# Kernel optimization log

Measured on AMD Instinct MI355X. Metric: run time of the kernel, lower is better.

The kernel has to match this reference:

```python
import jax, jax.numpy as jnp
import numpy as np

B, L, D, H = 2, 2048, 512, 8
DH = D // H
THRESHOLD = 0.1


def setup_inputs() -> dict:
    key = jax.random.key(0)
    ks = jax.random.split(key, 8)
    s = 0.02  # weight scale to keep activations sane
    return {
        "q_x": jax.random.normal(ks[0], (B, L, D), jnp.float32),
        "k_x": jax.random.normal(ks[1], (B, L, D), jnp.float32),
        "v_x": jax.random.normal(ks[2], (B, L, D), jnp.float32),
        "energy_coeffs": jax.random.normal(ks[3], (B, L, 16), jnp.float32),
        "Wq": jax.random.normal(ks[4], (D, D), jnp.float32) * s,
        "bq": jnp.zeros((D,), jnp.float32),
        "Wk": jax.random.normal(ks[5], (D, D), jnp.float32) * s,
        "bk": jnp.zeros((D,), jnp.float32),
        "Wv": jax.random.normal(ks[6], (D, D), jnp.float32) * s,
        "bv": jnp.zeros((D,), jnp.float32),
        "Wo": jax.random.normal(ks[7], (D, D), jnp.float32) * s,
        "bo": jnp.zeros((D,), jnp.float32),
    }


def reference(q_x, k_x, v_x, energy_coeffs, Wq, bq, Wk, bk, Wv, bv, Wo, bo):
    b, l, d = q_x.shape
    # QKV projections (torch Linear: x @ W.T + b), split heads -> [B,H,L,Dh]
    Q = (q_x @ Wq.T + bq).reshape(b, l, H, DH).transpose(0, 2, 1, 3)
    K = (k_x @ Wk.T + bk).reshape(b, -1, H, DH).transpose(0, 2, 1, 3)
    V = (v_x @ Wv.T + bv).reshape(b, -1, H, DH).transpose(0, 2, 1, 3)
    scores = jnp.einsum("bhqd,bhkd->bhqk", Q, K) / jnp.sqrt(jnp.float32(DH))
    # straight-through energy-based key mask
    energy = jnp.abs(energy_coeffs).mean(axis=-1)  # [B, Lk]
    soft = jax.nn.sigmoid((energy - THRESHOLD) * 10.0)
    hard = (energy > THRESHOLD).astype(q_x.dtype)
    mask_val = soft + jax.lax.stop_gradient(hard - soft)  # fwd=hard, grad=soft
    scores = scores + (1.0 - mask_val)[:, None, None, :] * (-1e9)
    attn = jax.nn.softmax(scores, axis=-1)
    out = jnp.einsum("bhqk,bhkd->bhqd", attn, V)
    out = out.transpose(0, 2, 1, 3).reshape(b, l, d)
    return out @ Wo.T + bo
```

## Files before the change

### kernel.cpp

```cpp
#include <hip/hip_runtime.h>
#include <stdint.h>

#define B_ 2
#define L_ 2048
#define D_ 512
#define H_ 8
#define DH_ 64

using frag8 = __attribute__((ext_vector_type(8))) short;
using bf4   = __attribute__((ext_vector_type(4))) short;
using f32x4 = __attribute__((ext_vector_type(4))) float;
using u32x4 = __attribute__((ext_vector_type(4))) unsigned int;

#define QSC 0.18033688011112042f

__device__ __forceinline__ unsigned short f2bf(float f) {
    unsigned int u = __float_as_uint(f);
    u += 0x7fffu + ((u >> 16) & 1u);
    return (unsigned short)(u >> 16);
}

__device__ __forceinline__ unsigned int cvtpk(float lo, float hi_) {
    unsigned int r;
    asm("v_cvt_pk_bf16_f32 %0, %1, %2" : "=v"(r) : "v"(lo), "v"(hi_));
    return r;
}

__device__ __forceinline__ void gl2lds16(const void* g, void* lds) {
    __builtin_amdgcn_global_load_lds((const __attribute__((address_space(1))) void*)g,
                                     (__attribute__((address_space(3))) void*)lds,
                                     16, 0, 0);
}

template<int N>
__device__ __forceinline__ void vmwait() {
    asm volatile("s_waitcnt vmcnt(%0)" :: "n"(N) : "memory");
}

__global__ __launch_bounds__(256) void cvt_mask_kernel(
    const float* __restrict__ qx, const float* __restrict__ kx, const float* __restrict__ vx,
    const float* __restrict__ Wq, const float* __restrict__ Wk, const float* __restrict__ Wv,
    const float* __restrict__ Wo, const float* __restrict__ ec,
    unsigned short* qb, unsigned short* kb, unsigned short* vb,
    unsigned short* wqb, unsigned short* wkb, unsigned short* wvb, unsigned short* wob,
    float* __restrict__ mk)
{
    const long NA = (long)B_ * L_ * D_;
    const long NW = (long)D_ * D_;
    const long total4 = (3 * NA + 4 * NW) / 4;
    long q4 = (long)blockIdx.x * 256 + threadIdx.x;
    if (q4 < total4) {
        long i = q4 * 4;
        const float* src; unsigned short* dst; long off;
        if (i < NA)            { src = qx; dst = qb; off = i; }
        else if (i < 2 * NA)   { src = kx; dst = kb; off = i - NA; }
        else if (i < 3 * NA)   { src = vx; dst = vb; off = i - 2 * NA; }
        else {
            long j = i - 3 * NA;
            int w = (int)(j / NW);
            off = j - (long)w * NW;
            src = (w == 0) ? Wq : (w == 1) ? Wk : (w == 2) ? Wv : Wo;
            dst = (w == 0) ? wqb : (w == 1) ? wkb : (w == 2) ? wvb : wob;
        }
        float4 v = *(const float4*)(src + off);
        ushort4 o;
        o.x = f2bf(v.x); o.y = f2bf(v.y); o.z = f2bf(v.z); o.w = f2bf(v.w);
        *(ushort4*)(dst + off) = o;
    } else {
        long i = q4 - total4;
        if (i < B_ * L_) {
            const float4* p4 = (const float4*)(ec + i * 16);
            float s = 0.0f;
#pragma unroll
            for (int j = 0; j < 4; ++j) {
                float4 v = p4[j];
                s += fabsf(v.x) + fabsf(v.y) + fabsf(v.z) + fabsf(v.w);
            }
            float energy = s * (1.0f / 16.0f);
            mk[i] = (energy > 0.1f) ? 0.0f : -1.0e9f;
        }
    }
}

struct GemmArgs { const unsigned short* A; const unsigned short* W;
                  const float* bias; void* C; int mode; };

template<int BM, int BN>
__global__ __launch_bounds__(256) void gemm_kernel(GemmArgs a0, GemmArgs a1, GemmArgs a2,
                                                   int M, int N, int K)
{
    const int nwg = gridDim.x * gridDim.y * gridDim.z;
    int flat = blockIdx.x + gridDim.x * (blockIdx.y + gridDim.y * blockIdx.z);
    int swz  = (flat & 7) * (nwg >> 3) + (flat >> 3);
    const int bx = swz % gridDim.x;
    int t2 = swz / gridDim.x;
    const int by = t2 % gridDim.y;
    const int bz = t2 / gridDim.y;

    GemmArgs ga = bz == 0 ? a0 : (bz == 1 ? a1 : a2);
    const unsigned short* __restrict__ A = ga.A;
    const unsigned short* __restrict__ W = ga.W;
    const float* __restrict__ bias = ga.bias;

    constexpr int MF = BM / 32;
    constexpr int NF = BN / 32;
    constexpr int NL = BM / 32 + BN / 32;

    __shared__ __align__(16) unsigned short As[2][BM * 64];
    __shared__ __align__(16) unsigned short Bs[2][BN * 64];

    const int tid  = threadIdx.x;
    const int lane = tid & 63;
    const int wave = tid >> 6;
    const int hi   = lane >> 4;
    const int ln   = lane & 15;
    const int wr   = wave >> 1;
    const int wc   = wave & 1;

    const long mBase = (long)by * BM;
    const long nBase = (long)bx * BN;

    f32x4 acc[MF][NF];
#pragma unroll
    for (int n = 0; n < NF; ++n) {
        float bv = bias[nBase + wc * (BN / 2) + n * 16 + ln];
#pragma unroll
        for (int m = 0; m < MF; ++m) acc[m][n] = (f32x4){bv, bv, bv, bv};
    }

#define GSTAGE(KT, BUF) do {                                                    \
    _Pragma("unroll")                                                           \
    for (int i_ = 0; i_ < BM / 32; ++i_) {                                      \
        int cl_ = i_ * 256 + tid;                                               \
        int r_ = cl_ >> 3, c_ = cl_ & 7, s_ = c_ ^ (r_ & 7);                    \
        gl2lds16(A + (mBase + r_) * K + (KT) + s_ * 8, As[BUF] + cl_ * 8);      \
    }                                                                           \
    _Pragma("unroll")                                                           \
    for (int i_ = 0; i_ < BN / 32; ++i_) {                                      \
        int cl_ = i_ * 256 + tid;                                               \
        int r_ = cl_ >> 3, c_ = cl_ & 7, s_ = c_ ^ (r_ & 7);                    \
        gl2lds16(W + (nBase + r_) * K + (KT) + s_ * 8, Bs[BUF] + cl_ * 8);      \
    }                                                                           \
} while (0)

    GSTAGE(0, 0);

    const int nk = K / 64;
    for (int t = 0; t < nk; ++t) {
        const int buf = t & 1;
        if (t + 1 < nk) {
            GSTAGE((t + 1) * 64, buf ^ 1);
            vmwait<NL>();
        } else {
            vmwait<0>();
        }
        __builtin_amdgcn_s_barrier();
        __builtin_amdgcn_sched_barrier(0);

        frag8 af[2][MF], bfr[2][NF];
#pragma unroll
        for (int kk = 0; kk < 2; ++kk) {
#pragma unroll
            for (int m = 0; m < MF; ++m) {
                int row = wr * (BM / 2) + m * 16 + ln;
                int c = (kk * 4 + hi) ^ (row & 7);
                af[kk][m] = *(const frag8*)(As[buf] + row * 64 + c * 8);
            }
#pragma unroll
            for (int n = 0; n < NF; ++n) {
                int row = wc * (BN / 2) + n * 16 + ln;
                int c = (kk * 4 + hi) ^ (row & 7);
                bfr[kk][n] = *(const frag8*)(Bs[buf] + row * 64 + c * 8);
            }
        }
        __builtin_amdgcn_s_setprio(1);
#pragma unroll
        for (int kk = 0; kk < 2; ++kk)
#pragma unroll
            for (int m = 0; m < MF; ++m)
#pragma unroll
                for (int n = 0; n < NF; ++n)
                    acc[m][n] = __builtin_amdgcn_mfma_f32_16x16x32_bf16(af[kk][m], bfr[kk][n], acc[m][n], 0, 0, 0);
        __builtin_amdgcn_s_setprio(0);
        __builtin_amdgcn_sched_barrier(0);
        __builtin_amdgcn_s_barrier();
    }
#undef GSTAGE

    const int mode = ga.mode;
#pragma unroll
    for (int m = 0; m < MF; ++m) {
#pragma unroll
        for (int n = 0; n < NF; ++n) {
            long col = nBase + wc * (BN / 2) + n * 16 + ln;
#pragma unroll
            for (int j = 0; j < 4; ++j) {
                long row = mBase + wr * (BM / 2) + m * 16 + hi * 4 + j;
                float v = acc[m][n][j];
                if (mode == 3) {
                    ((float*)ga.C)[row * N + col] = v;
                } else if (mode == 2) {
                    int dh = (int)col & 63;
                    int swv = ((dh & 7) << 1) | ((dh >> 3) & 1);
                    long nt = (row & ~63L) | (long)(((((int)(row >> 2)) & 15) ^ swv) << 2) | (row & 3);
                    ((unsigned short*)ga.C)[col * (long)(B_ * L_) + nt] = f2bf(v);
                } else {
                    if (mode == 1) v *= QSC;
                    ((unsigned short*)ga.C)[row * N + col] = f2bf(v);
                }
            }
        }
    }
}

__global__ __launch_bounds__(512, 4) void attn_kernel(
    const unsigned short* __restrict__ Qg, const unsigned short* __restrict__ Kg,
    const unsigned short* __restrict__ Vt, const float* __restrict__ mkg,
    unsigned short* __restrict__ Og)
{
    const int tid  = threadIdx.x;
    const int lane = tid & 63;
    const int wave = tid >> 6;
    const int grp  = wave >> 2;
    const int wq   = wave & 3;
    const int gtid = tid & 255;
    const int hi   = lane >> 4;
    const int ln   = lane & 15;

    const int bh = blockIdx.y;
    const int b  = bh >> 3, h = bh & 7;
    const unsigned short* Qb = Qg + ((long)b * L_) * D_ + h * DH_;
    const unsigned short* Kb = Kg + ((long)b * L_) * D_ + h * DH_;
    const unsigned short* Vb = Vt + (long)(h * DH_) * (B_ * L_) + (long)b * L_;
    const float* mkb = mkg + (long)b * L_;

    __shared__ __align__(16) char smem[65536];
    unsigned short* KsG = (unsigned short*)(smem + grp * 32768);
    unsigned short* VsG = (unsigned short*)(smem + grp * 32768 + 16384);

    const int q0 = blockIdx.x * 64 + wq * 16;

    frag8 qf[2];
#pragma unroll
    for (int ks = 0; ks < 2; ++ks)
        qf[ks] = *(const frag8*)(Qb + (long)(q0 + ln) * D_ + ks * 32 + hi * 8);

    const int sw  = ((ln & 7) << 1) | ((ln >> 3) & 1);
    const int sl0 = ((hi     ) ^ sw) << 2;
    const int sl1 = ((hi + 4 ) ^ sw) << 2;
    const int sl2 = ((hi + 8 ) ^ sw) << 2;
    const int sl3 = ((hi + 12) ^ sw) << 2;

#define STAGE(TT, BUF) do {                                                     \
    _Pragma("unroll")                                                           \
    for (int c2_ = 0; c2_ < 2; ++c2_) {                                         \
        int cl_ = c2_ * 256 + gtid;                                             \
        int r_ = cl_ >> 3, c_ = cl_ & 7;                                        \
        gl2lds16(Kb + (long)((TT) * 64 + r_) * D_ + ((c_ ^ (r_ & 7)) << 3),     \
                 KsG + (BUF) * 4096 + cl_ * 8);                                 \
        gl2lds16(Vb + (long)r_ * (B_ * L_) + (TT) * 64 + (c_ << 3),             \
                 VsG + (BUF) * 4096 + cl_ * 8);                                 \
    }                                                                           \
} while (0)

#define LOADM(TT, A0, A1, A2, A3) do {                                          \
    A0 = *(const f32x4*)(mkb + (TT) * 64 +      4 * hi);                        \
    A1 = *(const f32x4*)(mkb + (TT) * 64 + 16 + 4 * hi);                        \
    A2 = *(const f32x4*)(mkb + (TT) * 64 + 32 + 4 * hi);                        \
    A3 = *(const f32x4*)(mkb + (TT) * 64 + 48 + 4 * hi);                        \
} while (0)

    f32x4 o[4];
#pragma unroll
    for (int g = 0; g < 4; ++g) o[g] = (f32x4){0.f, 0.f, 0.f, 0.f};
    float m_run = -__builtin_inff();
    float l_run = 0.0f;
    f32x4 scp[4];
    f32x4 mc0, mc1, mc2, mc3;
    f32x4 mn0, mn1, mn2, mn3;

    auto SOFTPV = [&](const unsigned short* Vl) {
        float a0 = fmaxf(fmaxf(scp[0][0], scp[0][1]), fmaxf(scp[0][2], scp[0][3]));
        float a1 = fmaxf(fmaxf(scp[1][0], scp[1][1]), fmaxf(scp[1][2], scp[1][3]));
        float a2 = fmaxf(fmaxf(scp[2][0], scp[2][1]), fmaxf(scp[2][2], scp[2][3]));
        float a3 = fmaxf(fmaxf(scp[3][0], scp[3][1]), fmaxf(scp[3][2], scp[3][3]));
        float tl = fmaxf(fmaxf(a0, a1), fmaxf(a2, a3));
        float tA = __shfl_xor(tl, 16);
        float tB = __shfl_xor(tl, 32);
        float tC = __shfl_xor(tl, 48);
        float tmax = fmaxf(fmaxf(tl, tA), fmaxf(tB, tC));

        if (!__all(tmax <= m_run + 8.0f)) {
            float m_new = fmaxf(m_run, tmax);
            float alpha = __builtin_amdgcn_exp2f(m_run - m_new);
            float b0 = __shfl(alpha, 4 * hi + 0);
            float b1 = __shfl(alpha, 4 * hi + 1);
            float b2 = __shfl(alpha, 4 * hi + 2);
            float b3 = __shfl(alpha, 4 * hi + 3);
#pragma unroll
            for (int g = 0; g < 4; ++g) {
                o[g][0] *= b0; o[g][1] *= b1; o[g][2] *= b2; o[g][3] *= b3;
            }
            l_run *= alpha;
            m_run = m_new;
        }

        float p[16];
#pragma unroll
        for (int sh = 0; sh < 4; ++sh)
#pragma unroll
            for (int r = 0; r < 4; ++r)
                p[sh * 4 + r] = __builtin_amdgcn_exp2f(scp[sh][r] - m_run);
        float s01 = (p[0] + p[1]) + (p[2] + p[3]);
        float s23 = (p[4] + p[5]) + (p[6] + p[7]);
        float s45 = (p[8] + p[9]) + (p[10] + p[11]);
        float s67 = (p[12] + p[13]) + (p[14] + p[15]);
        float ps = (s01 + s23) + (s45 + s67);
        float pA = __shfl_xor(ps, 16);
        float pB = __shfl_xor(ps, 32);
        float pC = __shfl_xor(ps, 48);
        l_run += (ps + pA) + (pB + pC);

        union PU { u32x4 u; frag8 f; } p0u, p1u;
        p0u.u = (u32x4){cvtpk(p[0], p[1]),  cvtpk(p[2], p[3]),
                        cvtpk(p[4], p[5]),  cvtpk(p[6], p[7])};
        p1u.u = (u32x4){cvtpk(p[8], p[9]),  cvtpk(p[10], p[11]),
                        cvtpk(p[12], p[13]), cvtpk(p[14], p[15])};

        __builtin_amdgcn_s_setprio(1);
#pragma unroll
        for (int g = 0; g < 4; ++g) {
            int rowb = (g * 16 + ln) * 64;
            bf4 v0 = *(const bf4*)(Vl + rowb + sl0);
            bf4 v1 = *(const bf4*)(Vl + rowb + sl1);
            bf4 v2 = *(const bf4*)(Vl + rowb + sl2);
            bf4 v3 = *(const bf4*)(Vl + rowb + sl3);
            frag8 vf0 = __builtin_shufflevector(v0, v1, 0, 1, 2, 3, 4, 5, 6, 7);
            frag8 vf1 = __builtin_shufflevector(v2, v3, 0, 1, 2, 3, 4, 5, 6, 7);
            o[g] = __builtin_amdgcn_mfma_f32_16x16x32_bf16(p0u.f, vf0, o[g], 0, 0, 0);
            o[g] = __builtin_amdgcn_mfma_f32_16x16x32_bf16(p1u.f, vf1, o[g], 0, 0, 0);
        }
        __builtin_amdgcn_s_setprio(0);
    };

    auto QKSAVE = [&](const unsigned short* Kl) {
        scp[0] = mc0; scp[1] = mc1; scp[2] = mc2; scp[3] = mc3;
        __builtin_amdgcn_s_setprio(1);
#pragma unroll
        for (int sh = 0; sh < 4; ++sh) {
            int key = sh * 16 + ln;
#pragma unroll
            for (int ks = 0; ks < 2; ++ks) {
                frag8 kf = *(const frag8*)(Kl + key * 64 + (((ks * 4 + hi) ^ (ln & 7)) << 3));
                scp[sh] = __builtin_amdgcn_mfma_f32_16x16x32_bf16(kf, qf[ks], scp[sh], 0, 0, 0);
            }
        }
        __builtin_amdgcn_s_setprio(0);
    };

    STAGE(grp, 0);
    LOADM(grp, mc0, mc1, mc2, mc3);
    vmwait<0>();
    __builtin_amdgcn_s_barrier();
    __builtin_amdgcn_sched_barrier(0);
    STAGE(2 + grp, 1);
    LOADM(2 + grp, mn0, mn1, mn2, mn3);
    QKSAVE(KsG);

    for (int i = 1; i < 16; ++i) {
        const int buf = i & 1;
        SOFTPV(VsG + (buf ^ 1) * 4096);
        vmwait<0>();
        __builtin_amdgcn_s_barrier();
        __builtin_amdgcn_sched_barrier(0);
        if (i < 15) STAGE(2 * (i + 1) + grp, buf ^ 1);
        mc0 = mn0; mc1 = mn1; mc2 = mn2; mc3 = mn3;
        if (i < 15) LOADM(2 * (i + 1) + grp, mn0, mn1, mn2, mn3);
        QKSAVE(KsG + buf * 4096);
    }
    SOFTPV(VsG + 4096);
#undef STAGE
#undef LOADM

    __syncthreads();
    float* oX = (float*)smem;
    float* mX = (float*)(smem + 64 * 68 * 4);
    float* lX = mX + 64;

    if (grp == 1) {
#pragma unroll
        for (int g = 0; g < 4; ++g)
#pragma unroll
            for (int j = 0; j < 4; ++j)
                oX[(wq * 16 + 4 * hi + j) * 68 + g * 16 + ln] = o[g][j];
        if (hi == 0) { mX[wq * 16 + ln] = m_run; lX[wq * 16 + ln] = l_run; }
    }
    __syncthreads();
    if (grp == 0) {
#pragma unroll
        for (int j = 0; j < 4; ++j) {
            int q = 4 * hi + j;
            float mA = __shfl(m_run, q);
            float lA = __shfl(l_run, q);
            float mB = mX[wq * 16 + q];
            float lB = lX[wq * 16 + q];
            float mm = fmaxf(mA, mB);
            float aA = __builtin_amdgcn_exp2f(mA - mm);
            float aB = __builtin_amdgcn_exp2f(mB - mm);
            float inv = 1.0f / (lA * aA + lB * aB);
            aA *= inv; aB *= inv;
#pragma unroll
            for (int g = 0; g < 4; ++g) {
                float v = o[g][j] * aA + oX[(wq * 16 + q) * 68 + g * 16 + ln] * aB;
                long idx = ((long)b * L_ + q0 + q) * D_ + h * DH_ + g * 16 + ln;
                Og[idx] = f2bf(v);
            }
        }
    }
}

extern "C" void kernel_launch(void* const* d_in, const int* in_sizes, int n_in,
                              void* d_out, int out_size, void* d_ws, size_t ws_size,
                              hipStream_t stream)
{
    const float* qx = (const float*)d_in[0];
    const float* kx = (const float*)d_in[1];
    const float* vx = (const float*)d_in[2];
    const float* ec = (const float*)d_in[3];
    const float* Wq = (const float*)d_in[4];
    const float* bq = (const float*)d_in[5];
    const float* Wk = (const float*)d_in[6];
    const float* bk = (const float*)d_in[7];
    const float* Wv = (const float*)d_in[8];
    const float* bv = (const float*)d_in[9];
    const float* Wo = (const float*)d_in[10];
    const float* bo = (const float*)d_in[11];
    float* out = (float*)d_out;

    const long NA = (long)B_ * L_ * D_;
    const long NW = (long)D_ * D_;

    unsigned short* qb  = (unsigned short*)d_ws;
    unsigned short* kb  = qb + NA;
    unsigned short* vb  = kb + NA;
    unsigned short* wqb = vb + NA;
    unsigned short* wkb = wqb + NW;
    unsigned short* wvb = wkb + NW;
    unsigned short* wob = wvb + NW;
    unsigned short* Qp  = wob + NW;
    unsigned short* Kp  = Qp + NA;
    unsigned short* Vtp = Kp + NA;
    unsigned short* Ap  = qb;
    float*          mk  = (float*)(Vtp + NA);

    const long total4 = (3 * NA + 4 * NW) / 4;
    const long nblk = (total4 + B_ * L_ + 255) / 256;
    cvt_mask_kernel<<<dim3((unsigned)nblk), dim3(256), 0, stream>>>(
        qx, kx, vx, Wq, Wk, Wv, Wo, ec, qb, kb, vb, wqb, wkb, wvb, wob, mk);

    GemmArgs zq = {qb, wqb, bq, Qp, 1};
    GemmArgs zk = {kb, wkb, bk, Kp, 0};
    GemmArgs zv = {vb, wvb, bv, Vtp, 2};
    gemm_kernel<64, 64><<<dim3(8, 64, 3), dim3(256), 0, stream>>>(zq, zk, zv, B_ * L_, D_, D_);

    attn_kernel<<<dim3(L_ / 64, B_ * H_), dim3(512), 0, stream>>>(Qp, Kp, Vtp, mk, Ap);

    GemmArgs zo = {Ap, wob, bo, out, 3};
    gemm_kernel<32, 64><<<dim3(8, 128, 1), dim3(256), 0, stream>>>(zo, zo, zo, B_ * L_, D_, D_);
}
```

Measured before the change: 74.34 us.

## Fuse fp32-to-bf16 activation conversion into QKV GEMM and swizzle attention grid

The separate conversion pass over q_x/k_x/v_x is dropped. The QKV GEMM now loads fp32 activations straight into LDS with a 16-chunk XOR swizzle and packs them to bf16 when building fragments, which removes a full write and re-read of three activation tensors in bf16. The cost is doubled LDS footprint and global traffic for the A operand inside the GEMM, plus extra convert instructions in the inner loop. The attention kernel also remaps block indices with an 8-way XCD-style swizzle to improve K/V cache locality.

```diff
diff --git a/kernel.cpp b/kernel.cpp
--- a/kernel.cpp
+++ b/kernel.cpp
@@ -26,6 +26,13 @@
     return r;
 }
 
+__device__ __forceinline__ frag8 pk8(f32x4 lo, f32x4 hh) {
+    union { u32x4 u; frag8 f; } v;
+    v.u = (u32x4){cvtpk(lo[0], lo[1]), cvtpk(lo[2], lo[3]),
+                  cvtpk(hh[0], hh[1]), cvtpk(hh[2], hh[3])};
+    return v.f;
+}
+
 __device__ __forceinline__ void gl2lds16(const void* g, void* lds) {
     __builtin_amdgcn_global_load_lds((const __attribute__((address_space(1))) void*)g,
                                      (__attribute__((address_space(3))) void*)lds,
@@ -38,36 +45,25 @@
 }
 
 __global__ __launch_bounds__(256) void cvt_mask_kernel(
-    const float* __restrict__ qx, const float* __restrict__ kx, const float* __restrict__ vx,
     const float* __restrict__ Wq, const float* __restrict__ Wk, const float* __restrict__ Wv,
     const float* __restrict__ Wo, const float* __restrict__ ec,
-    unsigned short* qb, unsigned short* kb, unsigned short* vb,
     unsigned short* wqb, unsigned short* wkb, unsigned short* wvb, unsigned short* wob,
     float* __restrict__ mk)
 {
-    const long NA = (long)B_ * L_ * D_;
     const long NW = (long)D_ * D_;
-    const long total4 = (3 * NA + 4 * NW) / 4;
     long q4 = (long)blockIdx.x * 256 + threadIdx.x;
-    if (q4 < total4) {
+    if (q4 < NW) {
         long i = q4 * 4;
-        const float* src; unsigned short* dst; long off;
-        if (i < NA)            { src = qx; dst = qb; off = i; }
-        else if (i < 2 * NA)   { src = kx; dst = kb; off = i - NA; }
-        else if (i < 3 * NA)   { src = vx; dst = vb; off = i - 2 * NA; }
-        else {
-            long j = i - 3 * NA;
-            int w = (int)(j / NW);
-            off = j - (long)w * NW;
-            src = (w == 0) ? Wq : (w == 1) ? Wk : (w == 2) ? Wv : Wo;
-            dst = (w == 0) ? wqb : (w == 1) ? wkb : (w == 2) ? wvb : wob;
-        }
+        int w = (int)(i / NW);
+        long off = i - (long)w * NW;
+        const float* src = (w == 0) ? Wq : (w == 1) ? Wk : (w == 2) ? Wv : Wo;
+        unsigned short* dst = (w == 0) ? wqb : (w == 1) ? wkb : (w == 2) ? wvb : wob;
         float4 v = *(const float4*)(src + off);
         ushort4 o;
         o.x = f2bf(v.x); o.y = f2bf(v.y); o.z = f2bf(v.z); o.w = f2bf(v.w);
         *(ushort4*)(dst + off) = o;
     } else {
-        long i = q4 - total4;
+        long i = q4 - NW;
         if (i < B_ * L_) {
             const float4* p4 = (const float4*)(ec + i * 16);
             float s = 0.0f;
@@ -82,10 +78,10 @@
     }
 }
 
-struct GemmArgs { const unsigned short* A; const unsigned short* W;
+struct GemmArgs { const void* A; const unsigned short* W;
                   const float* bias; void* C; int mode; };
 
-template<int BM, int BN>
+template<int BM, int BN, int AF32>
 __global__ __launch_bounds__(256) void gemm_kernel(GemmArgs a0, GemmArgs a1, GemmArgs a2,
                                                    int M, int N, int K)
 {
@@ -98,16 +94,19 @@
     const int bz = t2 / gridDim.y;
 
     GemmArgs ga = bz == 0 ? a0 : (bz == 1 ? a1 : a2);
-    const unsigned short* __restrict__ A = ga.A;
+    const float* __restrict__ Af = (const float*)ga.A;
+    const unsigned short* __restrict__ Ab = (const unsigned short*)ga.A;
     const unsigned short* __restrict__ W = ga.W;
     const float* __restrict__ bias = ga.bias;
 
     constexpr int MF = BM / 32;
     constexpr int NF = BN / 32;
-    constexpr int NL = BM / 32 + BN / 32;
-
-    __shared__ __align__(16) unsigned short As[2][BM * 64];
+    constexpr int NL = (AF32 ? BM / 16 : BM / 32) + BN / 32;
+
+    __shared__ __align__(16) char sA[(size_t)2 * BM * 64 * (AF32 ? 4 : 2)];
     __shared__ __align__(16) unsigned short Bs[2][BN * 64];
+    float* AsF = (float*)sA;
+    unsigned short* As16 = (unsigned short*)sA;
 
     const int tid  = threadIdx.x;
     const int lane = tid & 63;
@@ -129,11 +128,22 @@
     }
 
 #define GSTAGE(KT, BUF) do {                                                    \
-    _Pragma("unroll")                                                           \
-    for (int i_ = 0; i_ < BM / 32; ++i_) {                                      \
-        int cl_ = i_ * 256 + tid;                                               \
-        int r_ = cl_ >> 3, c_ = cl_ & 7, s_ = c_ ^ (r_ & 7);                    \
-        gl2lds16(A + (mBase + r_) * K + (KT) + s_ * 8, As[BUF] + cl_ * 8);      \
+    if (AF32) {                                                                 \
+        _Pragma("unroll")                                                       \
+        for (int i_ = 0; i_ < BM / 16; ++i_) {           \
+            int cl_ = i_ * 256 + tid;                                           \
+            int r_ = cl_ >> 4, c_ = cl_ & 15, s_ = c_ ^ (r_ & 15);              \
+            gl2lds16(Af + (mBase + r_) * K + (KT) + s_ * 4,                     \
+                     AsF + ((BUF) * BM + r_) * 64 + (cl_ & 15) * 4);            \
+        }                                                                       \
+    } else {                                                                    \
+        _Pragma("unroll")                                                       \
+        for (int i_ = 0; i_ < BM / 32; ++i_) {                                  \
+            int cl_ = i_ * 256 + tid;                                           \
+            int r_ = cl_ >> 3, c_ = cl_ & 7, s_ = c_ ^ (r_ & 7);                \
+            gl2lds16(Ab + (mBase + r_) * K + (KT) + s_ * 8,                     \
+                     As16 + ((BUF) * BM + r_) * 64 + (cl_ & 7) * 8);            \
+        }                                                                       \
     }                                                                           \
     _Pragma("unroll")                                                           \
     for (int i_ = 0; i_ < BN / 32; ++i_) {                                      \
@@ -163,8 +173,17 @@
 #pragma unroll
             for (int m = 0; m < MF; ++m) {
                 int row = wr * (BM / 2) + m * 16 + ln;
-                int c = (kk * 4 + hi) ^ (row & 7);
-                af[kk][m] = *(const frag8*)(As[buf] + row * 64 + c * 8);
+                if (AF32) {
+                    int c0 = kk * 8 + hi * 2;
+                    int p0 = c0 ^ (row & 15);
+                    int p1 = (c0 + 1) ^ (row & 15);
+                    f32x4 lo = *(const f32x4*)(AsF + ((long)buf * BM + row) * 64 + p0 * 4);
+                    f32x4 hh = *(const f32x4*)(AsF + ((long)buf * BM + row) * 64 + p1 * 4);
+                    af[kk][m] = pk8(lo, hh);
+                } else {
+                    int c = (kk * 4 + hi) ^ (row & 7);
+                    af[kk][m] = *(const frag8*)(As16 + ((long)buf * BM + row) * 64 + c * 8);
+                }
             }
 #pragma unroll
             for (int n = 0; n < NF; ++n) {
@@ -227,7 +246,12 @@
     const int hi   = lane >> 4;
     const int ln   = lane & 15;
 
-    const int bh = blockIdx.y;
+    const int flat = blockIdx.x + gridDim.x * blockIdx.y;
+    const int nwg  = gridDim.x * gridDim.y;
+    const int s    = (flat & 7) * (nwg >> 3) + (flat >> 3);
+    const int qt   = s & (gridDim.x - 1);
+    const int bh   = s / gridDim.x;
+
     const int b  = bh >> 3, h = bh & 7;
     const unsigned short* Qb = Qg + ((long)b * L_) * D_ + h * DH_;
     const unsigned short* Kb = Kg + ((long)b * L_) * D_ + h * DH_;
@@ -238,7 +262,7 @@
     unsigned short* KsG = (unsigned short*)(smem + grp * 32768);
     unsigned short* VsG = (unsigned short*)(smem + grp * 32768 + 16384);
 
-    const int q0 = blockIdx.x * 64 + wq * 16;
+    const int q0 = qt * 64 + wq * 16;
 
     frag8 qf[2];
 #pragma unroll
@@ -440,31 +464,27 @@
     const long NA = (long)B_ * L_ * D_;
     const long NW = (long)D_ * D_;
 
-    unsigned short* qb  = (unsigned short*)d_ws;
-    unsigned short* kb  = qb + NA;
-    unsigned short* vb  = kb + NA;
-    unsigned short* wqb = vb + NA;
+    unsigned short* Ap  = (unsigned short*)d_ws;
+    unsigned short* wqb = Ap + NA;
     unsigned short* wkb = wqb + NW;
     unsigned short* wvb = wkb + NW;
     unsigned short* wob = wvb + NW;
     unsigned short* Qp  = wob + NW;
     unsigned short* Kp  = Qp + NA;
     unsigned short* Vtp = Kp + NA;
-    unsigned short* Ap  = qb;
     float*          mk  = (float*)(Vtp + NA);
 
-    const long total4 = (3 * NA + 4 * NW) / 4;
-    const long nblk = (total4 + B_ * L_ + 255) / 256;
+    const long nblk = (NW + B_ * L_ + 255) / 256;
     cvt_mask_kernel<<<dim3((unsigned)nblk), dim3(256), 0, stream>>>(
-        qx, kx, vx, Wq, Wk, Wv, Wo, ec, qb, kb, vb, wqb, wkb, wvb, wob, mk);
-
-    GemmArgs zq = {qb, wqb, bq, Qp, 1};
-    GemmArgs zk = {kb, wkb, bk, Kp, 0};
-    GemmArgs zv = {vb, wvb, bv, Vtp, 2};
-    gemm_kernel<64, 64><<<dim3(8, 64, 3), dim3(256), 0, stream>>>(zq, zk, zv, B_ * L_, D_, D_);
+        Wq, Wk, Wv, Wo, ec, wqb, wkb, wvb, wob, mk);
+
+    GemmArgs zq = {qx, wqb, bq, Qp, 1};
+    GemmArgs zk = {kx, wkb, bk, Kp, 0};
+    GemmArgs zv = {vx, wvb, bv, Vtp, 2};
+    gemm_kernel<64, 64, 1><<<dim3(8, 64, 3), dim3(256), 0, stream>>>(zq, zk, zv, B_ * L_, D_, D_);
 
     attn_kernel<<<dim3(L_ / 64, B_ * H_), dim3(512), 0, stream>>>(Qp, Kp, Vtp, mk, Ap);
 
     GemmArgs zo = {Ap, wob, bo, out, 3};
-    gemm_kernel<32, 64><<<dim3(8, 128, 1), dim3(256), 0, stream>>>(zo, zo, zo, B_ * L_, D_, D_);
-}
+    gemm_kernel<32, 64, 0><<<dim3(8, 128, 1), dim3(256), 0, stream>>>(zo, zo, zo, B_ * L_, D_, D_);
+}
```

Result: no change. 74.72 us (+0.5%).
